# Kernel optimization log

Hardware: AMD Instinct MI355X
Metric: run time of the kernel (lower is better)

## Reference

```python
import jax, jax.numpy as jnp
import numpy as np

SIZE = 512
N_STROKES = 8
N_SAMPLES = 32
STROKE_WIDTH = 0.04


def setup_inputs() -> dict:
    key = jax.random.key(0)
    k1, _ = jax.random.split(key)
    # control points seeded like torch.rand(...) * 0.6 + 0.2
    control_points = jax.random.uniform(k1, (N_STROKES, 4, 2), dtype=jnp.float32) * 0.6 + 0.2
    # pixel grid buffer: (x, y) coords in [0,1], row-major over (y, x)
    coords = jnp.linspace(0.0, 1.0, SIZE, dtype=jnp.float32)
    grid_y, grid_x = jnp.meshgrid(coords, coords, indexing="ij")
    pixel_grid = jnp.stack([grid_x, grid_y], axis=-1).reshape(-1, 2)  # (HW, 2)
    return {"control_points": control_points, "pixel_grid": pixel_grid}


def _bezier3_samples(curves, n_samples):
    # curves: (S, 4, 2) -> (S, n_samples, 2)
    ts = jnp.linspace(0.0, 1.0, n_samples, dtype=curves.dtype)
    t = ts[None, :, None]
    mt = 1.0 - t
    p0, p1, p2, p3 = (curves[:, k:k + 1, :] for k in range(4))
    return mt ** 3 * p0 + 3.0 * mt ** 2 * t * p1 + 3.0 * mt * t ** 2 * p2 + t ** 3 * p3


def reference(control_points, pixel_grid):
    # all_strokes(): symmetric=False, empty stroke_groups -> just clamp
    pts = jnp.clip(control_points, 0.0, 1.0)
    samples = _bezier3_samples(pts, N_SAMPLES).reshape(-1, 2)  # (P, 2), P = S*n_samples
    sharpness = float(N_SAMPLES) * 8.0
    # pairwise distances (HW, P) — soft-min via logsumexp over curve points
    diff = pixel_grid[:, None, :] - samples[None, :, :]          # (HW, P, 2)
    dist = jnp.sqrt(jnp.sum(diff * diff, axis=-1))               # (HW, P)
    min_dist = -jax.nn.logsumexp(-sharpness * dist, axis=-1) / sharpness  # (HW,)
    coverage = jax.nn.sigmoid((STROKE_WIDTH - min_dist) * (8.0 / STROKE_WIDTH))
    return (1.0 - coverage.reshape(SIZE, SIZE))[None]  # (1, H, W)
```

## Files before the change

kernel.cpp:

```cpp
#include <hip/hip_runtime.h>


#define SIZE 512
#define RADIUS 0.06f
#define FARCUT 0.1217f
#define HB 0.00684932f
#define HD 0.00968631f

__device__ __forceinline__ float clamp01(float x) {
    return fminf(fmaxf(x, 0.0f), 1.0f);
}
__device__ __forceinline__ float wave_min(float v) {
    #pragma unroll
    for (int m = 1; m < 64; m <<= 1) v = fminf(v, __shfl_xor(v, m));
    return v;
}
__device__ __forceinline__ float wave_max(float v) {
    #pragma unroll
    for (int m = 1; m < 64; m <<= 1) v = fmaxf(v, __shfl_xor(v, m));
    return v;
}

__global__ __launch_bounds__(64) void bezier_glyph_kernel(
        const float* __restrict__ cp,
        float* __restrict__ out)
{
    __shared__ float2 list1[260];
    __shared__ float2 list2[260];

    const int tid = threadIdx.x;
    const int b   = blockIdx.x;
    const int row_base = (b >> 6) << 3;
    const int col_base = (b & 63) << 3;
    const float inv = 1.0f / 511.0f;
    const float cx  = ((float)col_base + 3.5f) * inv;
    const float cy  = ((float)row_base + 3.5f) * inv;

    float sxv[4], syv[4], dc2v[4], bb2v[4];
    {
        const int s = tid >> 3;
        const float* p = cp + s * 8;
        const float x0 = clamp01(p[0]), y0 = clamp01(p[1]);
        const float x1 = clamp01(p[2]), y1 = clamp01(p[3]);
        const float x2 = clamp01(p[4]), y2 = clamp01(p[5]);
        const float x3 = clamp01(p[6]), y3 = clamp01(p[7]);
        #pragma unroll
        for (int r = 0; r < 4; ++r) {
            const int j    = ((tid << 2) + r) & 31;
            const float u  = (float)j * (1.0f / 31.0f);
            const float mu = 1.0f - u;
            const float w0 = mu * mu * mu;
            const float w1 = 3.0f * mu * mu * u;
            const float w2 = 3.0f * mu * u * u;
            const float w3 = u * u * u;
            const float sx = w0 * x0 + w1 * x1 + w2 * x2 + w3 * x3;
            const float sy = w0 * y0 + w1 * y1 + w2 * y2 + w3 * y3;
            sxv[r] = sx; syv[r] = sy;
            const float dcx = sx - cx, dcy = sy - cy;
            dc2v[r] = dcx * dcx + dcy * dcy;
            const float bx = fmaxf(fabsf(dcx) - HB, 0.0f);
            const float by = fmaxf(fabsf(dcy) - HB, 0.0f);
            bb2v[r] = bx * bx + by * by;
        }
    }

    const float Dc = __builtin_amdgcn_sqrtf(wave_min(
        fminf(fminf(dc2v[0], dc2v[1]), fminf(dc2v[2], dc2v[3]))));
    const float T1  = fminf(Dc, FARCUT + HD) + 2.0f * HD + 1e-4f;
    const float T1s = T1 * T1;

    const unsigned long long lt = (tid == 63) ? ~0ull >> 1
                                              : (1ull << tid) - 1ull;
    int n1 = 0;
    #pragma unroll
    for (int r = 0; r < 4; ++r) {
        const bool keep = (dc2v[r] <= T1s);
        const unsigned long long mk = __ballot(keep);
        if (keep)
            list1[n1 + (int)__popcll(mk & lt)] = make_float2(sxv[r], syv[r]);
        n1 += (int)__popcll(mk);
    }

    const int row = row_base + (tid >> 3);
    const int col = col_base + (tid & 7);

    if (n1 == 0) {
        out[row * SIZE + col] = 1.0f;
        return;
    }
    if (tid < 4) list1[n1 + tid] = make_float2(1e3f, 1e3f);
    __syncthreads();

    const float py = (float)row * inv;
    const float px = (float)col * inv;

    float m = 3e38f;
    const int n1r = (n1 + 3) & ~3;
    for (int k = 0; k < n1r; k += 4) {
        const float2 a = list1[k],     b2 = list1[k + 1];
        const float2 c = list1[k + 2], e  = list1[k + 3];
        float dx, dy;
        dx = px - a.x;  dy = py - a.y;  const float qa = fmaf(dx, dx, dy * dy);
        dx = px - b2.x; dy = py - b2.y; const float qb = fmaf(dx, dx, dy * dy);
        dx = px - c.x;  dy = py - c.y;  const float qc = fmaf(dx, dx, dy * dy);
        dx = px - e.x;  dy = py - e.y;  const float qe = fmaf(dx, dx, dy * dy);
        m = fminf(m, fminf(fminf(qa, qb), fminf(qc, qe)));
    }
    const float d   = __builtin_amdgcn_sqrtf(m);
    const float cap = fminf(d, FARCUT);

    const float dminw = wave_min(d);
    const float Tmax  = wave_max(cap);

    if (dminw > FARCUT) {
        out[row * SIZE + col] = 1.0f;
        return;
    }

    const float T2  = Tmax + RADIUS + 1e-4f;
    const float T2s = T2 * T2;
    int n2 = 0;
    #pragma unroll
    for (int r = 0; r < 4; ++r) {
        const bool keep = (bb2v[r] <= T2s);
        const unsigned long long mk = __ballot(keep);
        if (keep)
            list2[n2 + (int)__popcll(mk & lt)] = make_float2(sxv[r], syv[r]);
        n2 += (int)__popcll(mk);
    }
    if (tid < 4) list2[n2 + tid] = make_float2(1e3f, 1e3f);
    __syncthreads();

    const float C  = 369.3299304675766f;
    const float nC = -C;
    const float cd = C * d;
    float S = 0.0f;
    const int n2r = (n2 + 3) & ~3;
    for (int k = 0; k < n2r; k += 4) {
        const float2 a = list2[k],     b2 = list2[k + 1];
        const float2 c = list2[k + 2], e  = list2[k + 3];
        float dx, dy;
        dx = px - a.x;  dy = py - a.y;  const float qa = fmaf(dx, dx, dy * dy);
        dx = px - b2.x; dy = py - b2.y; const float qb = fmaf(dx, dx, dy * dy);
        dx = px - c.x;  dy = py - c.y;  const float qc = fmaf(dx, dx, dy * dy);
        dx = px - e.x;  dy = py - e.y;  const float qe = fmaf(dx, dx, dy * dy);
        S += __builtin_amdgcn_exp2f(fmaf(nC, __builtin_amdgcn_sqrtf(qa), cd))
           + __builtin_amdgcn_exp2f(fmaf(nC, __builtin_amdgcn_sqrtf(qb), cd))
           + __builtin_amdgcn_exp2f(fmaf(nC, __builtin_amdgcn_sqrtf(qc), cd))
           + __builtin_amdgcn_exp2f(fmaf(nC, __builtin_amdgcn_sqrtf(qe), cd));
    }

    const float md = d - __builtin_amdgcn_logf(S) * (1.0f / C);
    const float K  = 288.53900817779268f;
    out[row * SIZE + col] = __builtin_amdgcn_rcpf(
        1.0f + __builtin_amdgcn_exp2f((0.04f - md) * K));
}

extern "C" void kernel_launch(void* const* d_in, const int* in_sizes, int n_in,
                              void* d_out, int out_size, void* d_ws, size_t ws_size,
                              hipStream_t stream) {
    const float* cp = (const float*)d_in[0];
    float* out = (float*)d_out;
    bezier_glyph_kernel<<<dim3(4096), dim3(64), 0, stream>>>(cp, out);
}
```

Measured before the change: 59.37 us.

## Drop exact min-distance pass; use tile box lower bound as logsumexp shift

Removes the first culling pass, which built a candidate list and computed each pixel's exact nearest-sample distance. A single box-distance lower bound A for the whole 8x8 tile now drives both the early exit and the culling threshold, and also serves as the logsumexp stabilizing shift. This saves one shared-memory list, one barrier, one wave reduction and a full distance loop. It also evaluates the Bezier samples with Horner form. The cost is a looser culling threshold, so more samples may enter the exp loop, and the shift is no longer the exact per-pixel minimum.

```diff
diff --git a/kernel.cpp b/kernel.cpp
--- a/kernel.cpp
+++ b/kernel.cpp
@@ -15,18 +15,12 @@
     for (int m = 1; m < 64; m <<= 1) v = fminf(v, __shfl_xor(v, m));
     return v;
 }
-__device__ __forceinline__ float wave_max(float v) {
-    #pragma unroll
-    for (int m = 1; m < 64; m <<= 1) v = fmaxf(v, __shfl_xor(v, m));
-    return v;
-}
 
 __global__ __launch_bounds__(64) void bezier_glyph_kernel(
         const float* __restrict__ cp,
         float* __restrict__ out)
 {
-    __shared__ float2 list1[260];
-    __shared__ float2 list2[260];
+    __shared__ float2 list[260];
 
     const int tid = threadIdx.x;
     const int b   = blockIdx.x;
@@ -36,7 +30,7 @@
     const float cx  = ((float)col_base + 3.5f) * inv;
     const float cy  = ((float)row_base + 3.5f) * inv;
 
-    float sxv[4], syv[4], dc2v[4], bb2v[4];
+    float sxv[4], syv[4], bb2v[4];
     {
         const int s = tid >> 3;
         const float* p = cp + s * 8;
@@ -44,113 +38,73 @@
         const float x1 = clamp01(p[2]), y1 = clamp01(p[3]);
         const float x2 = clamp01(p[4]), y2 = clamp01(p[5]);
         const float x3 = clamp01(p[6]), y3 = clamp01(p[7]);
+        const float c1x = 3.0f * (x1 - x0);
+        const float c2x = 3.0f * (x0 - 2.0f * x1 + x2);
+        const float c3x = x3 - x0 + 3.0f * (x1 - x2);
+        const float c1y = 3.0f * (y1 - y0);
+        const float c2y = 3.0f * (y0 - 2.0f * y1 + y2);
+        const float c3y = y3 - y0 + 3.0f * (y1 - y2);
         #pragma unroll
         for (int r = 0; r < 4; ++r) {
             const int j    = ((tid << 2) + r) & 31;
             const float u  = (float)j * (1.0f / 31.0f);
-            const float mu = 1.0f - u;
-            const float w0 = mu * mu * mu;
-            const float w1 = 3.0f * mu * mu * u;
-            const float w2 = 3.0f * mu * u * u;
-            const float w3 = u * u * u;
-            const float sx = w0 * x0 + w1 * x1 + w2 * x2 + w3 * x3;
-            const float sy = w0 * y0 + w1 * y1 + w2 * y2 + w3 * y3;
+            const float sx = fmaf(fmaf(fmaf(c3x, u, c2x), u, c1x), u, x0);
+            const float sy = fmaf(fmaf(fmaf(c3y, u, c2y), u, c1y), u, y0);
             sxv[r] = sx; syv[r] = sy;
-            const float dcx = sx - cx, dcy = sy - cy;
-            dc2v[r] = dcx * dcx + dcy * dcy;
-            const float bx = fmaxf(fabsf(dcx) - HB, 0.0f);
-            const float by = fmaxf(fabsf(dcy) - HB, 0.0f);
-            bb2v[r] = bx * bx + by * by;
+            const float bx = fmaxf(fabsf(sx - cx) - HB, 0.0f);
+            const float by = fmaxf(fabsf(sy - cy) - HB, 0.0f);
+            bb2v[r] = fmaf(bx, bx, by * by);
         }
     }
 
-    const float Dc = __builtin_amdgcn_sqrtf(wave_min(
-        fminf(fminf(dc2v[0], dc2v[1]), fminf(dc2v[2], dc2v[3]))));
-    const float T1  = fminf(Dc, FARCUT + HD) + 2.0f * HD + 1e-4f;
-    const float T1s = T1 * T1;
-
-    const unsigned long long lt = (tid == 63) ? ~0ull >> 1
-                                              : (1ull << tid) - 1ull;
-    int n1 = 0;
-    #pragma unroll
-    for (int r = 0; r < 4; ++r) {
-        const bool keep = (dc2v[r] <= T1s);
-        const unsigned long long mk = __ballot(keep);
-        if (keep)
-            list1[n1 + (int)__popcll(mk & lt)] = make_float2(sxv[r], syv[r]);
-        n1 += (int)__popcll(mk);
-    }
+    const float A = __builtin_amdgcn_sqrtf(wave_min(
+        fminf(fminf(bb2v[0], bb2v[1]), fminf(bb2v[2], bb2v[3]))));
 
     const int row = row_base + (tid >> 3);
     const int col = col_base + (tid & 7);
 
-    if (n1 == 0) {
+    if (A > FARCUT) {
         out[row * SIZE + col] = 1.0f;
         return;
     }
-    if (tid < 4) list1[n1 + tid] = make_float2(1e3f, 1e3f);
+
+    const float T   = fminf(A + 2.0f * HD, FARCUT) + RADIUS + 1e-4f;
+    const float Ts  = T * T;
+    const unsigned long long lt = (1ull << tid) - 1ull;
+    int n = 0;
+    #pragma unroll
+    for (int r = 0; r < 4; ++r) {
+        const bool keep = (bb2v[r] <= Ts);
+        const unsigned long long mk = __ballot(keep);
+        if (keep)
+            list[n + (int)__popcll(mk & lt)] = make_float2(sxv[r], syv[r]);
+        n += (int)__popcll(mk);
+    }
+    if (tid < 4) list[n + tid] = make_float2(1e3f, 1e3f);
     __syncthreads();
 
     const float py = (float)row * inv;
     const float px = (float)col * inv;
-
-    float m = 3e38f;
-    const int n1r = (n1 + 3) & ~3;
-    for (int k = 0; k < n1r; k += 4) {
-        const float2 a = list1[k],     b2 = list1[k + 1];
-        const float2 c = list1[k + 2], e  = list1[k + 3];
+    const float C  = 369.3299304675766f;
+    const float nC = -C;
+    const float cA = C * A;
+    float S = 0.0f;
+    const int nr = (n + 3) & ~3;
+    for (int k = 0; k < nr; k += 4) {
+        const float2 a = list[k],     b2 = list[k + 1];
+        const float2 c = list[k + 2], e  = list[k + 3];
         float dx, dy;
         dx = px - a.x;  dy = py - a.y;  const float qa = fmaf(dx, dx, dy * dy);
         dx = px - b2.x; dy = py - b2.y; const float qb = fmaf(dx, dx, dy * dy);
         dx = px - c.x;  dy = py - c.y;  const float qc = fmaf(dx, dx, dy * dy);
         dx = px - e.x;  dy = py - e.y;  const float qe = fmaf(dx, dx, dy * dy);
-        m = fminf(m, fminf(fminf(qa, qb), fminf(qc, qe)));
-    }
-    const float d   = __builtin_amdgcn_sqrtf(m);
-    const float cap = fminf(d, FARCUT);
-
-    const float dminw = wave_min(d);
-    const float Tmax  = wave_max(cap);
-
-    if (dminw > FARCUT) {
-        out[row * SIZE + col] = 1.0f;
-        return;
+        S += __builtin_amdgcn_exp2f(fmaf(nC, __builtin_amdgcn_sqrtf(qa), cA))
+           + __builtin_amdgcn_exp2f(fmaf(nC, __builtin_amdgcn_sqrtf(qb), cA))
+           + __builtin_amdgcn_exp2f(fmaf(nC, __builtin_amdgcn_sqrtf(qc), cA))
+           + __builtin_amdgcn_exp2f(fmaf(nC, __builtin_amdgcn_sqrtf(qe), cA));
     }
 
-    const float T2  = Tmax + RADIUS + 1e-4f;
-    const float T2s = T2 * T2;
-    int n2 = 0;
-    #pragma unroll
-    for (int r = 0; r < 4; ++r) {
-        const bool keep = (bb2v[r] <= T2s);
-        const unsigned long long mk = __ballot(keep);
-        if (keep)
-            list2[n2 + (int)__popcll(mk & lt)] = make_float2(sxv[r], syv[r]);
-        n2 += (int)__popcll(mk);
-    }
-    if (tid < 4) list2[n2 + tid] = make_float2(1e3f, 1e3f);
-    __syncthreads();
-
-    const float C  = 369.3299304675766f;
-    const float nC = -C;
-    const float cd = C * d;
-    float S = 0.0f;
-    const int n2r = (n2 + 3) & ~3;
-    for (int k = 0; k < n2r; k += 4) {
-        const float2 a = list2[k],     b2 = list2[k + 1];
-        const float2 c = list2[k + 2], e  = list2[k + 3];
-        float dx, dy;
-        dx = px - a.x;  dy = py - a.y;  const float qa = fmaf(dx, dx, dy * dy);
-        dx = px - b2.x; dy = py - b2.y; const float qb = fmaf(dx, dx, dy * dy);
-        dx = px - c.x;  dy = py - c.y;  const float qc = fmaf(dx, dx, dy * dy);
-        dx = px - e.x;  dy = py - e.y;  const float qe = fmaf(dx, dx, dy * dy);
-        S += __builtin_amdgcn_exp2f(fmaf(nC, __builtin_amdgcn_sqrtf(qa), cd))
-           + __builtin_amdgcn_exp2f(fmaf(nC, __builtin_amdgcn_sqrtf(qb), cd))
-           + __builtin_amdgcn_exp2f(fmaf(nC, __builtin_amdgcn_sqrtf(qc), cd))
-           + __builtin_amdgcn_exp2f(fmaf(nC, __builtin_amdgcn_sqrtf(qe), cd));
-    }
-
-    const float md = d - __builtin_amdgcn_logf(S) * (1.0f / C);
+    const float md = A - __builtin_amdgcn_logf(S) * (1.0f / C);
     const float K  = 288.53900817779268f;
     out[row * SIZE + col] = __builtin_amdgcn_rcpf(
         1.0f + __builtin_amdgcn_exp2f((0.04f - md) * K));
```

After: 58.49 us. About the same (-1.5%).
